# Performance work log

Measured on AMD Instinct MI355X. Metric: run time of the kernel, lower is better.

## Reference

```python
import jax, jax.numpy as jnp
import numpy as np

CHUNK = 64
EPS = 1e-5


def segsum(a):
    # a: (..., T) -> (..., T, T) lower-triangular cumulative segment sums; -inf above diag
    T = a.shape[-1]
    cs = jnp.cumsum(a, axis=-1)
    ss = cs[..., :, None] - cs[..., None, :]
    mask = jnp.tril(jnp.ones((T, T), dtype=bool))
    return jnp.where(mask, ss, -jnp.inf)


def ssd(x, A, B, C, chunk):
    # x: (b, L, h, p), A: (b, L, h), B/C: (b, L, n)
    b, L, h, p = x.shape
    c = L // chunk
    x = x.reshape(b, c, chunk, h, p)
    A = A.reshape(b, c, chunk, h).transpose(0, 3, 1, 2)          # b h c l
    B = B.reshape(b, c, chunk, -1)                               # b c l n
    C = C.reshape(b, c, chunk, -1)                               # b c l n
    A_cum = jnp.cumsum(A, axis=-1)                               # b h c l
    Lmat = jnp.exp(segsum(A))                                    # b h c l l (causal decay)
    # intra-chunk (diagonal-block) output
    Y_diag = jnp.einsum('bcln,bcsn,bhcls,bcshp->bclhp', C, B, Lmat, x)
    # per-chunk states
    decay_states = jnp.exp(A_cum[..., -1:] - A_cum)              # b h c l
    states = jnp.einsum('bcln,bhcl,bclhp->bchpn', B, decay_states, x)
    states = jnp.concatenate([jnp.zeros_like(states[:, :1]), states], axis=1)  # b (c+1) h p n
    # inter-chunk recurrence via chunk-level segsum
    A_last = jnp.pad(A_cum[..., -1], ((0, 0), (0, 0), (1, 0)))   # b h (c+1)
    decay_chunk = jnp.exp(segsum(A_last))                        # b h (c+1) (c+1)
    new_states = jnp.einsum('bhzc,bchpn->bzhpn', decay_chunk, states)
    states, final = new_states[:, :-1], new_states[:, -1:]
    Y_off = jnp.einsum('bcln,bchpn,bhcl->bclhp', C, states, jnp.exp(A_cum))
    return (Y_diag + Y_off).reshape(b, L, h, p), final


def mamba2(x, W_in, conv_w, conv_b, dt_bias, A_log, D, norm_w, W_out):
    d_inner = norm_w.shape[0]
    nheads = dt_bias.shape[0]
    d_state = (conv_b.shape[0] - d_inner) // 2
    headdim = d_inner // nheads
    k_conv = conv_w.shape[0]
    b, L, _ = x.shape

    zxbcdt = x @ W_in                                            # (b, L, 2*d_inner+2*n+h)
    z = zxbcdt[..., :d_inner]
    xBC = zxbcdt[..., d_inner:2 * d_inner + 2 * d_state]
    dt = jax.nn.softplus(zxbcdt[..., 2 * d_inner + 2 * d_state:] + dt_bias)  # (b, L, h)
    A = -jnp.exp(A_log)                                          # (h,)

    # causal depthwise conv (zero init conv state == left-pad k_conv-1 zeros) + silu
    xp = jnp.pad(xBC, ((0, 0), (k_conv - 1, 0), (0, 0)))
    xBC = jax.lax.conv_general_dilated(
        xp, conv_w, (1,), 'VALID',
        dimension_numbers=('NWC', 'WIO', 'NWC'),
        feature_group_count=conv_b.shape[0])
    xBC = jax.nn.silu(xBC + conv_b)

    xs = xBC[..., :d_inner].reshape(b, L, nheads, headdim)       # (b, L, h, p)
    Bm = xBC[..., d_inner:d_inner + d_state]                     # (b, L, n)
    Cm = xBC[..., d_inner + d_state:]                            # (b, L, n)

    Y, _ = ssd(xs * dt[..., None], A * dt, Bm, Cm, CHUNK)
    Y = Y + xs * D                                               # D: (h, 1) broadcasts over p
    y = Y.reshape(b, L, d_inner)

    # gated RMSNorm
    y = y * jax.nn.silu(z)
    y = y * jax.lax.rsqrt(jnp.mean(y * y, axis=-1, keepdims=True) + EPS) * norm_w
    return y @ W_out


def setup_inputs():
    key = jax.random.key(0)
    ks = jax.random.split(key, 8)
    B, L, d_model = 2, 4096, 1024
    expand, d_state, k_conv, headdim = 2, 128, 4, 64
    d_inner = expand * d_model
    nheads = d_inner // headdim
    d_in_proj = 2 * d_inner + 2 * d_state + nheads
    conv_dim = d_inner + 2 * d_state
    return {
        'x': jax.random.normal(ks[0], (B, L, d_model), jnp.float32),
        'W_in': jax.random.normal(ks[1], (d_model, d_in_proj), jnp.float32) / np.sqrt(d_model).astype(np.float32),
        'conv_w': jax.random.normal(ks[2], (k_conv, 1, conv_dim), jnp.float32) / np.sqrt(k_conv).astype(np.float32),
        'conv_b': jnp.zeros((conv_dim,), jnp.float32),
        'dt_bias': jax.random.normal(ks[3], (nheads,), jnp.float32) * 0.5 - 2.0,
        'A_log': jnp.log(1.0 + 15.0 * jax.random.uniform(ks[4], (nheads,), jnp.float32)),
        'D': jax.random.normal(ks[5], (nheads, 1), jnp.float32),
        'norm_w': jnp.ones((d_inner,), jnp.float32),
        'W_out': jax.random.normal(ks[6], (d_inner, d_model), jnp.float32) / np.sqrt(d_inner).astype(np.float32),
    }


def reference(x, W_in, conv_w, conv_b, dt_bias, A_log, D, norm_w, W_out):
    return mamba2(x, W_in, conv_w, conv_b, dt_bias, A_log, D, norm_w, W_out)
```

## Files before the change

kernel.cpp:

```cpp
#include <hip/hip_runtime.h>
#include <hip/hip_fp16.h>

typedef _Float16 f16;
typedef _Float16 f16x4 __attribute__((ext_vector_type(4)));
typedef _Float16 f16x8 __attribute__((ext_vector_type(8)));
typedef float f32x4 __attribute__((ext_vector_type(4)));

#define DEV __device__ __forceinline__

constexpr int BB    = 2;
constexpr int LL    = 4096;
constexpr int DM    = 1024;
constexpr int DIN   = 2048;
constexpr int DST   = 128;
constexpr int NH    = 32;
constexpr int HD    = 64;
constexpr int NC    = 64;
constexpr int MROWS = BB * LL;
constexpr int NPROJ = 2*DIN + 2*DST + NH;
constexpr int NZ    = 2*DIN + 2*DST;
constexpr int CONVD = DIN + 2*DST;
constexpr int DT_OFF = 2*DIN + 2*DST;
constexpr int BOFF  = DIN;
constexpr int COFF  = DIN + DST;

DEV float silu_f(float v) { return v / (1.f + __expf(-v)); }

DEV void gload_lds16(const f16* gsrc, f16* lds_dst) {
  __builtin_amdgcn_global_load_lds(
      (const __attribute__((address_space(1))) void*)gsrc,
      (__attribute__((address_space(3))) void*)lds_dst, 16, 0, 0);
}

__global__ __launch_bounds__(256)
void tof16_kernel(const float* __restrict__ src, f16* __restrict__ dst, int n8) {
  int i = blockIdx.x * 256 + threadIdx.x;
  if (i >= n8) return;
  f32x4 a = *(const f32x4*)(src + (size_t)i*8);
  f32x4 b = *(const f32x4*)(src + (size_t)i*8 + 4);
  f16x8 o;
#pragma unroll
  for (int j = 0; j < 4; ++j) { o[j] = (f16)a[j]; o[4+j] = (f16)b[j]; }
  *(f16x8*)(dst + (size_t)i*8) = o;
}

__global__ __launch_bounds__(256)
void transpose_f32_to_f16(const float* __restrict__ src, f16* __restrict__ dst,
                          int K, int N, int srcLd) {
  __shared__ float tbuf[32][33];
  int n0 = blockIdx.x * 32, k0 = blockIdx.y * 32;
  int tx = threadIdx.x & 31, ty = threadIdx.x >> 5;
  for (int i = ty; i < 32; i += 8)
    tbuf[i][tx] = src[(size_t)(k0 + i)*srcLd + n0 + tx];
  __syncthreads();
  for (int i = ty; i < 32; i += 8)
    dst[(size_t)(n0 + i)*K + (k0 + tx)] = (f16)tbuf[tx][i];
}

template<bool C16>
__global__ __launch_bounds__(512, 2)
void gemm_p(const f16* __restrict__ A, const f16* __restrict__ Bt,
            void* __restrict__ Cp, int M, int N, int K, int ldc) {
  __shared__ f16 As3[3][256*32];
  __shared__ f16 Bs3[3][128*32];
  const int nbn = N >> 7;
  const int bm = blockIdx.x / nbn, bn = blockIdx.x % nbn;
  const int tid  = threadIdx.x;
  const int wave = tid >> 6, lane = tid & 63;
  const int lrow = lane & 15, kgrp = lane >> 4;
  const int wm = wave >> 1, wn = wave & 1;
  const int nt = K >> 5;

  const int rS = tid >> 2;
  const int cS = (tid & 3) * 8;
  const f16* Ag = A  + (size_t)(bm*256 + rS)*K + cS;
  const f16* Bg = Bt + (size_t)(bn*128 + rS)*K + cS;
  const int ldsOff = wave * 512;

  f32x4 acc[4][4] = {};

  auto STAGE = [&](int buf, int t) {
    const f16* a0 = Ag + (size_t)t*32;
    gload_lds16(a0,                 As3[buf] + ldsOff);
    gload_lds16(a0 + (size_t)128*K, As3[buf] + ldsOff + 4096);
    gload_lds16(Bg + (size_t)t*32,  Bs3[buf] + ldsOff);
  };

  STAGE(0, 0);
  if (nt > 1) {
    STAGE(1, 1);
    asm volatile("s_waitcnt vmcnt(3)" ::: "memory");
  } else {
    asm volatile("s_waitcnt vmcnt(0)" ::: "memory");
  }
  __builtin_amdgcn_s_barrier();
  __builtin_amdgcn_sched_barrier(0);

  for (int t = 0; t < nt; ++t) {
    const int cur = t % 3;
    if (t + 2 < nt) STAGE((t + 2) % 3, t + 2);
    const f16* Ab = As3[cur];
    const f16* Bb = Bs3[cur];
    f16x8 bf[4];
#pragma unroll
    for (int n = 0; n < 4; ++n)
      bf[n] = *(const f16x8*)(Bb + (wn*64 + n*16 + lrow)*32 + kgrp*8);
#pragma unroll
    for (int m = 0; m < 4; ++m) {
      f16x8 af = *(const f16x8*)(Ab + (wm*64 + m*16 + lrow)*32 + kgrp*8);
#pragma unroll
      for (int n = 0; n < 4; ++n)
        acc[m][n] = __builtin_amdgcn_mfma_f32_16x16x32_f16(af, bf[n], acc[m][n], 0, 0, 0);
    }
    if (t + 1 < nt) {
      if (t + 2 < nt) asm volatile("s_waitcnt vmcnt(3)" ::: "memory");
      else            asm volatile("s_waitcnt vmcnt(0)" ::: "memory");
      __builtin_amdgcn_s_barrier();
      __builtin_amdgcn_sched_barrier(0);
    }
  }

  int crow0 = bm*256 + wm*64, ccol0 = bn*128 + wn*64;
#pragma unroll
  for (int m = 0; m < 4; ++m)
#pragma unroll
    for (int n = 0; n < 4; ++n) {
      int r0 = crow0 + m*16 + (lane >> 4)*4;
      int c0 = ccol0 + n*16 + (lane & 15);
#pragma unroll
      for (int r = 0; r < 4; ++r) {
        if constexpr (C16) {
          f16* C = (f16*)Cp;
          C[(size_t)(r0 + r)*ldc + c0] = (f16)acc[m][n][r];
        } else {
          float* C = (float*)Cp;
          C[(size_t)(r0 + r)*ldc + c0] = acc[m][n][r];
        }
      }
    }
}

__global__ __launch_bounds__(256)
void dt_kernel(const float* __restrict__ x, const float* __restrict__ Win,
               const float* __restrict__ dt_bias, float* __restrict__ dt) {
  __shared__ float xs[64][132];
  __shared__ float ws[128][32];
  int r0 = blockIdx.x * 64;
  int t = threadIdx.x;
  int r = t >> 2, c0 = (t & 3) * 8;
  float acc[8] = {};
  for (int kt = 0; kt < 1024; kt += 128) {
    __syncthreads();
#pragma unroll
    for (int i = 0; i < 8; ++i) {
      int idx4 = t + i*256;
      int rr = idx4 >> 5, c4 = (idx4 & 31) * 4;
      *(f32x4*)&xs[rr][c4] = *(const f32x4*)(x + (size_t)(r0 + rr)*1024 + kt + c4);
    }
#pragma unroll
    for (int i = 0; i < 4; ++i) {
      int idx4 = t + i*256;
      int rr = idx4 >> 3, c4 = (idx4 & 7) * 4;
      *(f32x4*)&ws[rr][c4] = *(const f32x4*)(Win + (size_t)(kt + rr)*NPROJ + DT_OFF + c4);
    }
    __syncthreads();
#pragma unroll 8
    for (int k = 0; k < 128; ++k) {
      float xv = xs[r][k];
      f32x4 w0 = *(const f32x4*)&ws[k][c0];
      f32x4 w1 = *(const f32x4*)&ws[k][c0 + 4];
#pragma unroll
      for (int j = 0; j < 4; ++j) { acc[j] += xv * w0[j]; acc[4+j] += xv * w1[j]; }
    }
  }
#pragma unroll
  for (int j = 0; j < 8; ++j) {
    float v = acc[j] + dt_bias[c0 + j];
    float sp = (v > 20.f) ? v : log1pf(__expf(v));
    dt[(size_t)(r0 + r)*NH + c0 + j] = sp;
  }
}

__global__ __launch_bounds__(256)
void conv_kernel(const f16* __restrict__ zxh, const float* __restrict__ cw,
                 const float* __restrict__ cb, f16* __restrict__ out) {
  int i = blockIdx.x * 256 + threadIdx.x;
  int row = i / (CONVD/8);
  int c8  = (i - row*(CONVD/8)) * 8;
  int lb = row & (LL - 1);
  f32x4 a0 = *(const f32x4*)(cb + c8);
  f32x4 a1 = *(const f32x4*)(cb + c8 + 4);
#pragma unroll
  for (int j = 0; j < 4; ++j) {
    int lsrc = lb - 3 + j;
    if (lsrc >= 0) {
      f16x8 v = *(const f16x8*)(zxh + (size_t)(row - 3 + j)*NZ + BOFF + c8);
      f32x4 w0 = *(const f32x4*)(cw + j*CONVD + c8);
      f32x4 w1 = *(const f32x4*)(cw + j*CONVD + c8 + 4);
#pragma unroll
      for (int jj = 0; jj < 4; ++jj) {
        a0[jj] += (float)v[jj]   * w0[jj];
        a1[jj] += (float)v[4+jj] * w1[jj];
      }
    }
  }
  f16x8 o;
#pragma unroll
  for (int jj = 0; jj < 4; ++jj) {
    o[jj]   = (f16)silu_f(a0[jj]);
    o[4+jj] = (f16)silu_f(a1[jj]);
  }
  *(f16x8*)(out + (size_t)row*CONVD + c8) = o;
}

__global__ __launch_bounds__(256)
void acum_kernel(const float* __restrict__ dt, const float* __restrict__ A_log,
                 float* __restrict__ Acum) {
  int bc = blockIdx.x;
  int wave = threadIdx.x >> 6, lane = threadIdx.x & 63;
  int row = bc*64 + lane;
  for (int hh = 0; hh < 8; ++hh) {
    int h = wave*8 + hh;
    float A = -__expf(A_log[h]);
    float v = A * dt[(size_t)row*NH + h];
#pragma unroll
    for (int off = 1; off < 64; off <<= 1) {
      float u = __shfl_up(v, off);
      if (lane >= off) v += u;
    }
    Acum[((size_t)bc*NH + h)*64 + lane] = v;
  }
}

__global__ __launch_bounds__(256)
void gbuf_kernel(const f16* __restrict__ xbc, f16* __restrict__ G) {
  __shared__ float Cs[64][128];
  __shared__ float Bsm[64][128];
  int bc = blockIdx.x;
  int row0 = bc * 64;
  int t = threadIdx.x;
#pragma unroll
  for (int i = 0; i < 4; ++i) {
    int idx = t + i*256;
    int r = idx >> 4, c8 = (idx & 15) * 8;
    f16x8 cv = *(const f16x8*)(xbc + (size_t)(row0 + r)*CONVD + COFF + c8);
    f16x8 bv = *(const f16x8*)(xbc + (size_t)(row0 + r)*CONVD + BOFF + c8);
    f32x4 c0v = {(float)cv[0], (float)cv[1], (float)cv[2], (float)cv[3]};
    f32x4 c1v = {(float)cv[4], (float)cv[5], (float)cv[6], (float)cv[7]};
    f32x4 b0v = {(float)bv[0], (float)bv[1], (float)bv[2], (float)bv[3]};
    f32x4 b1v = {(float)bv[4], (float)bv[5], (float)bv[6], (float)bv[7]};
    *(f32x4*)&Cs[r][c8]      = c0v;  *(f32x4*)&Cs[r][c8 + 4]  = c1v;
    *(f32x4*)&Bsm[r][c8]     = b0v;  *(f32x4*)&Bsm[r][c8 + 4] = b1v;
  }
  __syncthreads();
  int l0 = (t >> 4)*4, s0 = (t & 15)*4;
  float acc[4][4] = {};
  for (int n4 = 0; n4 < 128; n4 += 4) {
    f32x4 cv[4], bv[4];
#pragma unroll
    for (int i = 0; i < 4; ++i) cv[i] = *(const f32x4*)&Cs[l0 + i][n4];
#pragma unroll
    for (int j = 0; j < 4; ++j) bv[j] = *(const f32x4*)&Bsm[s0 + j][n4];
#pragma unroll
    for (int i = 0; i < 4; ++i)
#pragma unroll
      for (int j = 0; j < 4; ++j)
        acc[i][j] += cv[i][0]*bv[j][0] + cv[i][1]*bv[j][1] + cv[i][2]*bv[j][2] + cv[i][3]*bv[j][3];
  }
#pragma unroll
  for (int i = 0; i < 4; ++i) {
    f16x4 v = {(f16)acc[i][0], (f16)acc[i][1], (f16)acc[i][2], (f16)acc[i][3]};
    *(f16x4*)(G + ((size_t)bc*64 + l0 + i)*64 + s0) = v;
  }
}

__global__ __launch_bounds__(256)
void ssd_a_kernel(const f16* __restrict__ xbc, const float* __restrict__ dtb,
                  const f16* __restrict__ Gg, const float* __restrict__ Acum,
                  f16* __restrict__ Ybuf, f16* __restrict__ states) {
  __shared__ union {
    struct { f16 XdT[64][72]; f16 Gt[64][72]; f16 BT[128][72]; } s;
    float Yl[64][68];
    float Sl[64][132];
  } u;
  __shared__ float ac[64], dts[64];
  int bc = blockIdx.x >> 5, h = blockIdx.x & 31;
  int row0 = bc*64, t = threadIdx.x;
  if (t < 64) {
    ac[t]  = Acum[((size_t)bc*NH + h)*64 + t];
    dts[t] = dtb[(size_t)(row0 + t)*NH + h];
  }
  __syncthreads();
  float ac63 = ac[63];
#pragma unroll
  for (int i = 0; i < 2; ++i) {
    int idx = t + i*256; int l = idx >> 3, p8 = (idx & 7)*8;
    f16x8 v = *(const f16x8*)(xbc + (size_t)(row0 + l)*CONVD + h*HD + p8);
    float d = dts[l];
#pragma unroll
    for (int j = 0; j < 8; ++j) u.s.XdT[p8 + j][l] = (f16)((float)v[j]*d);
  }
#pragma unroll
  for (int i = 0; i < 4; ++i) {
    int idx = t + i*256; int l = idx >> 4, n8 = (idx & 15)*8;
    f16x8 v = *(const f16x8*)(xbc + (size_t)(row0 + l)*CONVD + BOFF + n8);
    float dl = __expf(ac63 - ac[l]);
#pragma unroll
    for (int j = 0; j < 8; ++j) u.s.BT[n8 + j][l] = (f16)((float)v[j]*dl);
  }
#pragma unroll
  for (int i = 0; i < 2; ++i) {
    int idx = t + i*256; int l = idx >> 3, s8 = (idx & 7)*8;
    f16x8 g = *(const f16x8*)(Gg + (size_t)bc*4096 + l*64 + s8);
    float al = ac[l];
    f16x8 o;
#pragma unroll
    for (int j = 0; j < 8; ++j) {
      int s = s8 + j;
      o[j] = (l >= s) ? (f16)((float)g[j] * __expf(al - ac[s])) : (f16)0.f;
    }
    *(f16x8*)&u.s.Gt[l][s8] = o;
  }
  __syncthreads();
  int wave = t >> 6, lane = t & 63;
  int lrow = lane & 15, kgrp = lane >> 4;
  f32x4 yacc[4] = {};
  f32x4 sacc[8] = {};
#pragma unroll
  for (int kk = 0; kk < 64; kk += 32) {
    f16x8 afy = *(const f16x8*)&u.s.Gt[wave*16 + lrow][kk + kgrp*8];
    f16x8 afs = *(const f16x8*)&u.s.XdT[wave*16 + lrow][kk + kgrp*8];
#pragma unroll
    for (int n = 0; n < 4; ++n) {
      f16x8 bf = *(const f16x8*)&u.s.XdT[n*16 + lrow][kk + kgrp*8];
      yacc[n] = __builtin_amdgcn_mfma_f32_16x16x32_f16(afy, bf, yacc[n], 0, 0, 0);
    }
#pragma unroll
    for (int n = 0; n < 8; ++n) {
      f16x8 bf = *(const f16x8*)&u.s.BT[n*16 + lrow][kk + kgrp*8];
      sacc[n] = __builtin_amdgcn_mfma_f32_16x16x32_f16(afs, bf, sacc[n], 0, 0, 0);
    }
  }
  __syncthreads();
#pragma unroll
  for (int n = 0; n < 4; ++n)
#pragma unroll
    for (int r = 0; r < 4; ++r)
      u.Yl[wave*16 + kgrp*4 + r][n*16 + lrow] = yacc[n][r];
  __syncthreads();
#pragma unroll
  for (int i = 0; i < 2; ++i) {
    int idx = t + i*256; int l = idx >> 3, p8 = (idx & 7)*8;
    f16x8 o;
#pragma unroll
    for (int j = 0; j < 8; ++j) o[j] = (f16)u.Yl[l][p8 + j];
    *(f16x8*)(Ybuf + (size_t)(row0 + l)*DIN + h*HD + p8) = o;
  }
  __syncthreads();
#pragma unroll
  for (int n = 0; n < 8; ++n)
#pragma unroll
    for (int r = 0; r < 4; ++r)
      u.Sl[wave*16 + kgrp*4 + r][n*16 + lrow] = sacc[n][r];
  __syncthreads();
  size_t sb = ((size_t)bc*NH + h)*8192;
#pragma unroll
  for (int i = 0; i < 4; ++i) {
    int idx = t + i*256; int p = idx >> 4, n8 = (idx & 15)*8;
    f16x8 o;
#pragma unroll
    for (int j = 0; j < 8; ++j) o[j] = (f16)u.Sl[p][n8 + j];
    *(f16x8*)(states + sb + (size_t)p*128 + n8) = o;
  }
}

__global__ __launch_bounds__(256)
void scan_kernel(f16* __restrict__ states, const float* __restrict__ Acum) {
  int bid = blockIdx.x;
  int bh = bid >> 3, pgrp = bid & 7;
  int b = bh >> 5, h = bh & 31;
  int t = threadIdx.x;
  int p = pgrp*8 + (t >> 5), n4 = (t & 31) * 4;
  size_t off = (size_t)p*128 + n4;
  f32x4 carry = {0.f, 0.f, 0.f, 0.f};
  for (int c = 0; c < NC; ++c) {
    size_t base = ((size_t)(b*NC + c)*NH + h)*8192;
    f16x4 cv = *(f16x4*)(states + base + off);
    f16x4 st;
#pragma unroll
    for (int j = 0; j < 4; ++j) st[j] = (f16)carry[j];
    *(f16x4*)(states + base + off) = st;
    float tc = __expf(Acum[((size_t)(b*NC + c)*NH + h)*64 + 63]);
#pragma unroll
    for (int j = 0; j < 4; ++j) carry[j] = carry[j]*tc + (float)cv[j];
  }
}

__global__ __launch_bounds__(256)
void yoff_kernel(const f16* __restrict__ xbc, const f16* __restrict__ zxh,
                 const f16* __restrict__ states, const float* __restrict__ Acum,
                 const float* __restrict__ Dp, f16* __restrict__ Ybuf) {
  __shared__ union {
    struct { f16 Ch[64][136]; f16 Sin[64][136]; } s;
    float Yl[64][68];
  } u;
  __shared__ float eac[64];
  int bc = blockIdx.x >> 5, h = blockIdx.x & 31;
  int row0 = bc*64, t = threadIdx.x;
  if (t < 64) eac[t] = __expf(Acum[((size_t)bc*NH + h)*64 + t]);
  size_t sb = ((size_t)bc*NH + h)*8192;
#pragma unroll
  for (int i = 0; i < 4; ++i) {
    int idx = t + i*256; int r = idx >> 4, c8 = (idx & 15)*8;
    *(f16x8*)&u.s.Ch[r][c8]  = *(const f16x8*)(xbc + (size_t)(row0 + r)*CONVD + COFF + c8);
    *(f16x8*)&u.s.Sin[r][c8] = *(const f16x8*)(states + sb + (size_t)r*128 + c8);
  }
  __syncthreads();
  int wave = t >> 6, lane = t & 63;
  int lrow = lane & 15, kgrp = lane >> 4;
  f32x4 acc[4] = {};
#pragma unroll
  for (int kk = 0; kk < 128; kk += 32) {
    f16x8 af = *(const f16x8*)&u.s.Ch[wave*16 + lrow][kk + kgrp*8];
#pragma unroll
    for (int n = 0; n < 4; ++n) {
      f16x8 bf = *(const f16x8*)&u.s.Sin[n*16 + lrow][kk + kgrp*8];
      acc[n] = __builtin_amdgcn_mfma_f32_16x16x32_f16(af, bf, acc[n], 0, 0, 0);
    }
  }
  __syncthreads();
#pragma unroll
  for (int n = 0; n < 4; ++n)
#pragma unroll
    for (int r = 0; r < 4; ++r)
      u.Yl[wave*16 + kgrp*4 + r][n*16 + lrow] = acc[n][r];
  __syncthreads();
  float Dh = Dp[h];
#pragma unroll
  for (int i = 0; i < 2; ++i) {
    int idx = t + i*256; int l = idx >> 3, p8 = (idx & 7)*8;
    int row = row0 + l;
    f16x8 yd = *(const f16x8*)(Ybuf + (size_t)row*DIN + h*HD + p8);
    f16x8 zh = *(const f16x8*)(zxh + (size_t)row*NZ + h*HD + p8);
    f16x8 xs = *(const f16x8*)(xbc + (size_t)row*CONVD + h*HD + p8);
    float e = eac[l];
    f16x8 o;
#pragma unroll
    for (int j = 0; j < 8; ++j) {
      float yv = (float)yd[j] + e*u.Yl[l][p8 + j] + (float)xs[j]*Dh;
      o[j] = (f16)(yv * silu_f((float)zh[j]));
    }
    *(f16x8*)(Ybuf + (size_t)row*DIN + h*HD + p8) = o;
  }
}

__global__ __launch_bounds__(256)
void rms_kernel(const f16* __restrict__ yg, const float* __restrict__ nw,
                f16* __restrict__ yh) {
  __shared__ float red[4];
  int row = blockIdx.x, t = threadIdx.x;
  f16x8 v = *(const f16x8*)(yg + (size_t)row*DIN + t*8);
  float f[8];
  float ss = 0.f;
#pragma unroll
  for (int j = 0; j < 8; ++j) { f[j] = (float)v[j]; ss += f[j]*f[j]; }
#pragma unroll
  for (int off = 32; off > 0; off >>= 1) ss += __shfl_down(ss, off);
  if ((t & 63) == 0) red[t >> 6] = ss;
  __syncthreads();
  float tot = red[0] + red[1] + red[2] + red[3];
  float sc = rsqrtf(tot * (1.f/2048.f) + 1e-5f);
  f32x4 w0 = *(const f32x4*)(nw + t*8);
  f32x4 w1 = *(const f32x4*)(nw + t*8 + 4);
  f16x8 o;
#pragma unroll
  for (int j = 0; j < 4; ++j) {
    o[j]   = (f16)(f[j]   * sc * w0[j]);
    o[4+j] = (f16)(f[4+j] * sc * w1[j]);
  }
  *(f16x8*)(yh + (size_t)row*DIN + t*8) = o;
}

extern "C" void kernel_launch(void* const* d_in, const int* in_sizes, int n_in,
                              void* d_out, int out_size, void* d_ws, size_t ws_size,
                              hipStream_t stream) {
  const float* x       = (const float*)d_in[0];
  const float* W_in    = (const float*)d_in[1];
  const float* conv_w  = (const float*)d_in[2];
  const float* conv_b  = (const float*)d_in[3];
  const float* dt_bias = (const float*)d_in[4];
  const float* A_log   = (const float*)d_in[5];
  const float* Dp      = (const float*)d_in[6];
  const float* norm_w  = (const float*)d_in[7];
  const float* W_out   = (const float*)d_in[8];

  constexpr size_t WS_NEED = 213909504;
  if (ws_size < WS_NEED) return;

  char* w = (char*)d_ws;
  f16*   states = (f16*)(w + 0);
  f16*   winT   = (f16*)(w + 0);
  f16*   yh     = (f16*)(w + 0);
  f16*   xh     = (f16*)(w + 33554432);
  f16*   woutT  = (f16*)(w + 33554432);
  f16*   zxh    = (f16*)(w + 67108864);
  f16*   xbcc   = (f16*)(w + 138412032);
  f16*   Ybuf   = (f16*)(w + 176160768);
  float* dtb    = (float*)(w + 209715200);
  float* Acum   = (float*)(w + 210763776);
  f16*   Gg     = (f16*)(w + 211812352);

  tof16_kernel<<<4096, 256, 0, stream>>>(x, xh, MROWS*DM/8);
  transpose_f32_to_f16<<<dim3(NZ/32, DM/32), 256, 0, stream>>>(W_in, winT, DM, NZ, NPROJ);
  gemm_p<true><<<(MROWS/256)*(NZ/128), 512, 0, stream>>>(xh, winT, zxh, MROWS, NZ, DM, NZ);
  dt_kernel<<<MROWS/64, 256, 0, stream>>>(x, W_in, dt_bias, dtb);
  conv_kernel<<<MROWS*(CONVD/8)/256, 256, 0, stream>>>(zxh, conv_w, conv_b, xbcc);
  acum_kernel<<<BB*NC, 256, 0, stream>>>(dtb, A_log, Acum);
  gbuf_kernel<<<BB*NC, 256, 0, stream>>>(xbcc, Gg);
  ssd_a_kernel<<<BB*NC*NH, 256, 0, stream>>>(xbcc, dtb, Gg, Acum, Ybuf, states);
  scan_kernel<<<BB*NH*8, 256, 0, stream>>>(states, Acum);
  yoff_kernel<<<BB*NC*NH, 256, 0, stream>>>(xbcc, zxh, states, Acum, Dp, Ybuf);
  transpose_f32_to_f16<<<dim3(DM/32, DIN/32), 256, 0, stream>>>(W_out, woutT, DIN, DM, DM);
  rms_kernel<<<MROWS, 256, 0, stream>>>(Ybuf, norm_w, yh);
  gemm_p<false><<<(MROWS/256)*(DM/128), 512, 0, stream>>>(yh, woutT, d_out, MROWS, DM, DIN, DM);
}
```

Baseline: 436.2 us.

## Templatize GEMM tiles, swizzle LDS layout, enlarge input-projection tile

Turns the fixed 256x128 GEMM into a template over block and wave tile shapes. It also adds an XOR swizzle on the LDS column groups to cut bank conflicts on fragment reads. The input projection now uses 256x256 tiles with 8 waves, and the output projection uses 256x128 tiles with 4 waves, each wave owning 128x64. The aim is more data reuse per loaded tile and fewer LDS conflicts, at the cost of more accumulator registers and possibly lower occupancy or fewer blocks for the wave count.

```diff
diff --git a/kernel.cpp b/kernel.cpp
--- a/kernel.cpp
+++ b/kernel.cpp
@@ -57,39 +57,57 @@
     dst[(size_t)(n0 + i)*K + (k0 + tx)] = (f16)tbuf[tx][i];
 }
 
-template<bool C16>
-__global__ __launch_bounds__(512, 2)
-void gemm_p(const f16* __restrict__ A, const f16* __restrict__ Bt,
+template<int BM, int BN, int WM_, int WN_, bool C16>
+__global__ __launch_bounds__(WM_*WN_*64, 2)
+void gemm_t(const f16* __restrict__ A, const f16* __restrict__ Bt,
             void* __restrict__ Cp, int M, int N, int K, int ldc) {
-  __shared__ f16 As3[3][256*32];
-  __shared__ f16 Bs3[3][128*32];
-  const int nbn = N >> 7;
+  constexpr int THREADS = WM_*WN_*64;
+  constexpr int WTM = BM/WM_, WTN = BN/WN_;
+  constexpr int FM = WTM/16, FN = WTN/16;
+  constexpr int LA = BM*4/THREADS, LB = BN*4/THREADS;
+  constexpr int L = LA + LB;
+  __shared__ f16 As[3][BM*32];
+  __shared__ f16 Bs[3][BN*32];
+  const int nbn = N / BN;
   const int bm = blockIdx.x / nbn, bn = blockIdx.x % nbn;
-  const int tid  = threadIdx.x;
+  const int tid = threadIdx.x;
   const int wave = tid >> 6, lane = tid & 63;
   const int lrow = lane & 15, kgrp = lane >> 4;
-  const int wm = wave >> 1, wn = wave & 1;
+  const int wm = wave / WN_, wn = wave % WN_;
   const int nt = K >> 5;
-
-  const int rS = tid >> 2;
-  const int cS = (tid & 3) * 8;
-  const f16* Ag = A  + (size_t)(bm*256 + rS)*K + cS;
-  const f16* Bg = Bt + (size_t)(bn*128 + rS)*K + cS;
-  const int ldsOff = wave * 512;
-
-  f32x4 acc[4][4] = {};
+  const int bcol8 = (kgrp ^ ((lrow ^ (lrow >> 2)) & 3)) * 8;
+
+  const f16* aptr[LA];
+  const f16* bptr[LB];
+#pragma unroll
+  for (int i = 0; i < LA; ++i) {
+    int s = tid + i*THREADS, row = s >> 2;
+    int g = (s & 3) ^ ((row ^ (row >> 2)) & 3);
+    aptr[i] = A + (size_t)(bm*BM + row)*K + g*8;
+  }
+#pragma unroll
+  for (int i = 0; i < LB; ++i) {
+    int s = tid + i*THREADS, row = s >> 2;
+    int g = (s & 3) ^ ((row ^ (row >> 2)) & 3);
+    bptr[i] = Bt + (size_t)(bn*BN + row)*K + g*8;
+  }
+
+  f32x4 acc[FM][FN] = {};
 
   auto STAGE = [&](int buf, int t) {
-    const f16* a0 = Ag + (size_t)t*32;
-    gload_lds16(a0,                 As3[buf] + ldsOff);
-    gload_lds16(a0 + (size_t)128*K, As3[buf] + ldsOff + 4096);
-    gload_lds16(Bg + (size_t)t*32,  Bs3[buf] + ldsOff);
+#pragma unroll
+    for (int i = 0; i < LA; ++i)
+      gload_lds16(aptr[i] + (size_t)t*32, As[buf] + (wave*64 + i*THREADS)*8);
+#pragma unroll
+    for (int i = 0; i < LB; ++i)
+      gload_lds16(bptr[i] + (size_t)t*32, Bs[buf] + (wave*64 + i*THREADS)*8);
   };
 
   STAGE(0, 0);
   if (nt > 1) {
     STAGE(1, 1);
-    asm volatile("s_waitcnt vmcnt(3)" ::: "memory");
+    if constexpr (L == 4) asm volatile("s_waitcnt vmcnt(4)" ::: "memory");
+    else                  asm volatile("s_waitcnt vmcnt(6)" ::: "memory");
   } else {
     asm volatile("s_waitcnt vmcnt(0)" ::: "memory");
   }
@@ -99,32 +117,36 @@
   for (int t = 0; t < nt; ++t) {
     const int cur = t % 3;
     if (t + 2 < nt) STAGE((t + 2) % 3, t + 2);
-    const f16* Ab = As3[cur];
-    const f16* Bb = Bs3[cur];
-    f16x8 bf[4];
-#pragma unroll
-    for (int n = 0; n < 4; ++n)
-      bf[n] = *(const f16x8*)(Bb + (wn*64 + n*16 + lrow)*32 + kgrp*8);
-#pragma unroll
-    for (int m = 0; m < 4; ++m) {
-      f16x8 af = *(const f16x8*)(Ab + (wm*64 + m*16 + lrow)*32 + kgrp*8);
-#pragma unroll
-      for (int n = 0; n < 4; ++n)
+    const f16* Ab = As[cur];
+    const f16* Bb = Bs[cur];
+    f16x8 bf[FN];
+#pragma unroll
+    for (int n = 0; n < FN; ++n)
+      bf[n] = *(const f16x8*)(Bb + (wn*WTN + n*16 + lrow)*32 + bcol8);
+#pragma unroll
+    for (int m = 0; m < FM; ++m) {
+      f16x8 af = *(const f16x8*)(Ab + (wm*WTM + m*16 + lrow)*32 + bcol8);
+#pragma unroll
+      for (int n = 0; n < FN; ++n)
         acc[m][n] = __builtin_amdgcn_mfma_f32_16x16x32_f16(af, bf[n], acc[m][n], 0, 0, 0);
     }
     if (t + 1 < nt) {
-      if (t + 2 < nt) asm volatile("s_waitcnt vmcnt(3)" ::: "memory");
-      else            asm volatile("s_waitcnt vmcnt(0)" ::: "memory");
+      if (t + 2 < nt) {
+        if constexpr (L == 4) asm volatile("s_waitcnt vmcnt(4)" ::: "memory");
+        else                  asm volatile("s_waitcnt vmcnt(6)" ::: "memory");
+      } else {
+        asm volatile("s_waitcnt vmcnt(0)" ::: "memory");
+      }
       __builtin_amdgcn_s_barrier();
       __builtin_amdgcn_sched_barrier(0);
     }
   }
 
-  int crow0 = bm*256 + wm*64, ccol0 = bn*128 + wn*64;
-#pragma unroll
-  for (int m = 0; m < 4; ++m)
-#pragma unroll
-    for (int n = 0; n < 4; ++n) {
+  int crow0 = bm*BM + wm*WTM, ccol0 = bn*BN + wn*WTN;
+#pragma unroll
+  for (int m = 0; m < FM; ++m)
+#pragma unroll
+    for (int n = 0; n < FN; ++n) {
       int r0 = crow0 + m*16 + (lane >> 4)*4;
       int c0 = ccol0 + n*16 + (lane & 15);
 #pragma unroll
@@ -512,7 +534,7 @@
 
   tof16_kernel<<<4096, 256, 0, stream>>>(x, xh, MROWS*DM/8);
   transpose_f32_to_f16<<<dim3(NZ/32, DM/32), 256, 0, stream>>>(W_in, winT, DM, NZ, NPROJ);
-  gemm_p<true><<<(MROWS/256)*(NZ/128), 512, 0, stream>>>(xh, winT, zxh, MROWS, NZ, DM, NZ);
+  gemm_t<256,256,2,4,true><<<(MROWS/256)*(NZ/256), 512, 0, stream>>>(xh, winT, zxh, MROWS, NZ, DM, NZ);
   dt_kernel<<<MROWS/64, 256, 0, stream>>>(x, W_in, dt_bias, dtb);
   conv_kernel<<<MROWS*(CONVD/8)/256, 256, 0, stream>>>(zxh, conv_w, conv_b, xbcc);
   acum_kernel<<<BB*NC, 256, 0, stream>>>(dtb, A_log, Acum);
@@ -522,5 +544,5 @@
   yoff_kernel<<<BB*NC*NH, 256, 0, stream>>>(xbcc, zxh, states, Acum, Dp, Ybuf);
   transpose_f32_to_f16<<<dim3(DM/32, DIN/32), 256, 0, stream>>>(W_out, woutT, DIN, DM, DM);
   rms_kernel<<<MROWS, 256, 0, stream>>>(Ybuf, norm_w, yh);
-  gemm_p<false><<<(MROWS/256)*(DM/128), 512, 0, stream>>>(yh, woutT, d_out, MROWS, DM, DIN, DM);
-}
+  gemm_t<256,128,2,2,false><<<(MROWS/256)*(DM/128), 256, 0, stream>>>(yh, woutT, d_out, MROWS, DM, DIN, DM);
+}
```

After: 480.9 us. 1.1x slower.

## Rewrite projection GEMMs with BK=64, swizzled LDS, and ping-pong split pipeline

Applied to the files above, without the earlier changes.

Replaces the GEMM kernel used for both projections with a variant that uses a K-tile of 64, an XOR-swizzled LDS layout to avoid bank conflicts, and a loop split into two half-steps. Each half-step interleaves LDS fragment reads and async global-to-LDS staging with an MFMA burst run at raised wave priority. The aim is to hide memory latency better and cut barrier overhead per K element. In exchange, LDS use roughly doubles, which forces one block per CU (launch bounds 512,1), so occupancy falls.

```diff
diff --git a/kernel.cpp b/kernel.cpp
--- a/kernel.cpp
+++ b/kernel.cpp
@@ -58,38 +58,72 @@
 }
 
 template<bool C16>
-__global__ __launch_bounds__(512, 2)
-void gemm_p(const f16* __restrict__ A, const f16* __restrict__ Bt,
-            void* __restrict__ Cp, int M, int N, int K, int ldc) {
-  __shared__ f16 As3[3][256*32];
-  __shared__ f16 Bs3[3][128*32];
-  const int nbn = N >> 7;
+__global__ __launch_bounds__(512, 1)
+void gemm_8p(const f16* __restrict__ A, const f16* __restrict__ Bt,
+             void* __restrict__ Cp, int M, int N, int K, int ldc) {
+  constexpr int BM = 256, BN = 128, BK = 64;
+  constexpr int AF16 = BM*BK;
+  constexpr int BF16 = BN*BK;
+  constexpr int BUF  = AF16 + BF16;
+  __shared__ f16 smem[3*BUF];
+  const int nbn = N / BN;
   const int bm = blockIdx.x / nbn, bn = blockIdx.x % nbn;
-  const int tid  = threadIdx.x;
+  const int tid = threadIdx.x;
   const int wave = tid >> 6, lane = tid & 63;
   const int lrow = lane & 15, kgrp = lane >> 4;
   const int wm = wave >> 1, wn = wave & 1;
-  const int nt = K >> 5;
-
-  const int rS = tid >> 2;
-  const int cS = (tid & 3) * 8;
-  const f16* Ag = A  + (size_t)(bm*256 + rS)*K + cS;
-  const f16* Bg = Bt + (size_t)(bn*128 + rS)*K + cS;
-  const int ldsOff = wave * 512;
+  const int nt = K / BK;
+
+  const f16* aSrc[4]; const f16* bSrc[2];
+  int dA[4], dB[2];
+#pragma unroll
+  for (int i = 0; i < 4; ++i) {
+    int Lb = ((i*8 + wave)*64 + lane) * 16;
+    int sw = Lb ^ (((Lb >> 9) & 1) << 5);
+    int row = sw >> 7, colf = (sw & 127) >> 1;
+    aSrc[i] = A + (size_t)(bm*BM + row)*K + colf;
+    dA[i] = (i*8 + wave) * 512;
+  }
+#pragma unroll
+  for (int i = 0; i < 2; ++i) {
+    int Lb = ((i*8 + wave)*64 + lane) * 16;
+    int sw = Lb ^ (((Lb >> 9) & 1) << 5);
+    int row = sw >> 7, colf = (sw & 127) >> 1;
+    bSrc[i] = Bt + (size_t)(bn*BN + row)*K + colf;
+    dB[i] = (i*8 + wave) * 512;
+  }
+  int aIdx[4][2], bIdx[4][2];
+#pragma unroll
+  for (int m = 0; m < 4; ++m)
+#pragma unroll
+    for (int kk = 0; kk < 2; ++kk) {
+      int r = wm*64 + m*16 + lrow;
+      int off = r*128 + kk*64 + kgrp*16;
+      aIdx[m][kk] = (off ^ (((off >> 9) & 1) << 5)) >> 1;
+      r = wn*64 + m*16 + lrow;
+      off = r*128 + kk*64 + kgrp*16;
+      bIdx[m][kk] = (off ^ (((off >> 9) & 1) << 5)) >> 1;
+    }
 
   f32x4 acc[4][4] = {};
 
-  auto STAGE = [&](int buf, int t) {
-    const f16* a0 = Ag + (size_t)t*32;
-    gload_lds16(a0,                 As3[buf] + ldsOff);
-    gload_lds16(a0 + (size_t)128*K, As3[buf] + ldsOff + 4096);
-    gload_lds16(Bg + (size_t)t*32,  Bs3[buf] + ldsOff);
+  auto STAGE = [&](int buf, int t, int s) {
+    f16* Ab = smem + buf*BUF;
+    f16* Bb = Ab + AF16;
+    if (s == 0) {
+      gload_lds16(aSrc[0] + (size_t)t*BK, Ab + dA[0]);
+      gload_lds16(aSrc[1] + (size_t)t*BK, Ab + dA[1]);
+      gload_lds16(bSrc[0] + (size_t)t*BK, Bb + dB[0]);
+    } else {
+      gload_lds16(aSrc[2] + (size_t)t*BK, Ab + dA[2]);
+      gload_lds16(aSrc[3] + (size_t)t*BK, Ab + dA[3]);
+      gload_lds16(bSrc[1] + (size_t)t*BK, Bb + dB[1]);
+    }
   };
 
-  STAGE(0, 0);
-  if (nt > 1) {
-    STAGE(1, 1);
-    asm volatile("s_waitcnt vmcnt(3)" ::: "memory");
+  STAGE(0, 0, 0); STAGE(0, 0, 1);
+  if (nt > 1) { STAGE(1, 1, 0); STAGE(1, 1, 1);
+    asm volatile("s_waitcnt vmcnt(6)" ::: "memory");
   } else {
     asm volatile("s_waitcnt vmcnt(0)" ::: "memory");
   }
@@ -98,29 +132,50 @@
 
   for (int t = 0; t < nt; ++t) {
     const int cur = t % 3;
-    if (t + 2 < nt) STAGE((t + 2) % 3, t + 2);
-    const f16* Ab = As3[cur];
-    const f16* Bb = Bs3[cur];
-    f16x8 bf[4];
-#pragma unroll
-    for (int n = 0; n < 4; ++n)
-      bf[n] = *(const f16x8*)(Bb + (wn*64 + n*16 + lrow)*32 + kgrp*8);
-#pragma unroll
-    for (int m = 0; m < 4; ++m) {
-      f16x8 af = *(const f16x8*)(Ab + (wm*64 + m*16 + lrow)*32 + kgrp*8);
+    const f16* Ab = smem + cur*BUF;
+    const f16* Bb = Ab + AF16;
+    f16x8 af[4], bf[4];
+#pragma unroll
+    for (int m = 0; m < 4; ++m) af[m] = *(const f16x8*)(Ab + aIdx[m][0]);
+#pragma unroll
+    for (int n = 0; n < 4; ++n) bf[n] = *(const f16x8*)(Bb + bIdx[n][0]);
+    if (t + 2 < nt) STAGE((t + 2) % 3, t + 2, 0);
+    __builtin_amdgcn_s_barrier();
+    asm volatile("s_waitcnt lgkmcnt(0)" ::: "memory");
+    __builtin_amdgcn_sched_barrier(0);
+    __builtin_amdgcn_s_setprio(1);
+#pragma unroll
+    for (int m = 0; m < 4; ++m)
 #pragma unroll
       for (int n = 0; n < 4; ++n)
-        acc[m][n] = __builtin_amdgcn_mfma_f32_16x16x32_f16(af, bf[n], acc[m][n], 0, 0, 0);
-    }
+        acc[m][n] = __builtin_amdgcn_mfma_f32_16x16x32_f16(af[m], bf[n], acc[m][n], 0, 0, 0);
+    __builtin_amdgcn_s_setprio(0);
+    __builtin_amdgcn_s_barrier();
+    __builtin_amdgcn_sched_barrier(0);
+#pragma unroll
+    for (int m = 0; m < 4; ++m) af[m] = *(const f16x8*)(Ab + aIdx[m][1]);
+#pragma unroll
+    for (int n = 0; n < 4; ++n) bf[n] = *(const f16x8*)(Bb + bIdx[n][1]);
+    if (t + 2 < nt) STAGE((t + 2) % 3, t + 2, 1);
     if (t + 1 < nt) {
-      if (t + 2 < nt) asm volatile("s_waitcnt vmcnt(3)" ::: "memory");
+      if (t + 2 < nt) asm volatile("s_waitcnt vmcnt(6)" ::: "memory");
       else            asm volatile("s_waitcnt vmcnt(0)" ::: "memory");
-      __builtin_amdgcn_s_barrier();
-      __builtin_amdgcn_sched_barrier(0);
-    }
-  }
-
-  int crow0 = bm*256 + wm*64, ccol0 = bn*128 + wn*64;
+    }
+    __builtin_amdgcn_s_barrier();
+    asm volatile("s_waitcnt lgkmcnt(0)" ::: "memory");
+    __builtin_amdgcn_sched_barrier(0);
+    __builtin_amdgcn_s_setprio(1);
+#pragma unroll
+    for (int m = 0; m < 4; ++m)
+#pragma unroll
+      for (int n = 0; n < 4; ++n)
+        acc[m][n] = __builtin_amdgcn_mfma_f32_16x16x32_f16(af[m], bf[n], acc[m][n], 0, 0, 0);
+    __builtin_amdgcn_s_setprio(0);
+    __builtin_amdgcn_s_barrier();
+    __builtin_amdgcn_sched_barrier(0);
+  }
+
+  int crow0 = bm*BM + wm*64, ccol0 = bn*BN + wn*64;
 #pragma unroll
   for (int m = 0; m < 4; ++m)
 #pragma unroll
@@ -512,7 +567,7 @@
 
   tof16_kernel<<<4096, 256, 0, stream>>>(x, xh, MROWS*DM/8);
   transpose_f32_to_f16<<<dim3(NZ/32, DM/32), 256, 0, stream>>>(W_in, winT, DM, NZ, NPROJ);
-  gemm_p<true><<<(MROWS/256)*(NZ/128), 512, 0, stream>>>(xh, winT, zxh, MROWS, NZ, DM, NZ);
+  gemm_8p<true><<<(MROWS/256)*(NZ/128), 512, 0, stream>>>(xh, winT, zxh, MROWS, NZ, DM, NZ);
   dt_kernel<<<MROWS/64, 256, 0, stream>>>(x, W_in, dt_bias, dtb);
   conv_kernel<<<MROWS*(CONVD/8)/256, 256, 0, stream>>>(zxh, conv_w, conv_b, xbcc);
   acum_kernel<<<BB*NC, 256, 0, stream>>>(dtb, A_log, Acum);
@@ -522,5 +577,5 @@
   yoff_kernel<<<BB*NC*NH, 256, 0, stream>>>(xbcc, zxh, states, Acum, Dp, Ybuf);
   transpose_f32_to_f16<<<dim3(DM/32, DIN/32), 256, 0, stream>>>(W_out, woutT, DIN, DM, DM);
   rms_kernel<<<MROWS, 256, 0, stream>>>(Ybuf, norm_w, yh);
-  gemm_p<false><<<(MROWS/256)*(DM/128), 512, 0, stream>>>(yh, woutT, d_out, MROWS, DM, DIN, DM);
-}
+  gemm_8p<false><<<(MROWS/256)*(DM/128), 512, 0, stream>>>(yh, woutT, d_out, MROWS, DM, DIN, DM);
+}
```

Result: no change. 439.4 us (+0.7%).
